# Performance work log

Hardware: AMD Instinct MI355X
Metric: run time of the kernel (lower is better)

Reference implementation:

```python
import jax, jax.numpy as jnp
import numpy as np


def _mlp2(x, w1, b1, w2, b2):
    # two-linear MLP with tanh after each layer (Sequential(MLP, activation))
    h = jnp.tanh(x @ w1.T + b1)
    return jnp.tanh(h @ w2.T + b2)


def setup_inputs() -> dict:
    key = jax.random.key(0)
    ks = jax.random.split(key, 12)
    N, K, D, H, C = 20000, 32, 128, 128, 64
    s = 0.1
    return {
        "z": jax.random.normal(ks[0], (N, D), jnp.float32),
        "z_": jax.random.normal(ks[1], (N, K, D), jnp.float32),
        "cur_w1": s * jax.random.normal(ks[2], (H, D), jnp.float32),
        "cur_b1": jax.random.uniform(ks[3], (H,), jnp.float32, -0.1, 0.1),
        "cur_w2": s * jax.random.normal(ks[4], (H, H), jnp.float32),
        "cur_b2": jax.random.uniform(ks[5], (H,), jnp.float32, -0.1, 0.1),
        "nbr_w1": s * jax.random.normal(ks[6], (H, 2 * D), jnp.float32),
        "nbr_b1": jax.random.uniform(ks[7], (H,), jnp.float32, -0.1, 0.1),
        "nbr_w2": s * jax.random.normal(ks[8], (H, H), jnp.float32),
        "nbr_b2": jax.random.uniform(ks[9], (H,), jnp.float32, -0.1, 0.1),
        "out_w": s * jax.random.normal(ks[10], (C, 2 * H), jnp.float32),
        "out_b": jax.random.uniform(ks[11], (C,), jnp.float32, -0.1, 0.1),
    }


def reference(z, z_, cur_w1, cur_b1, cur_w2, cur_b2,
              nbr_w1, nbr_b1, nbr_w2, nbr_b2, out_w, out_b):
    N, K, D = z_.shape
    # current-node branch: [N, H]
    v = _mlp2(z, cur_w1, cur_b1, cur_w2, cur_b2)
    # neighbor branch: repeat z over K, concat with z_ -> [N, K, 2D]
    zc = jnp.concatenate([jnp.broadcast_to(z[:, None, :], (N, K, D)), z_], axis=2)
    vn = _mlp2(zc, nbr_w1, nbr_b1, nbr_w2, nbr_b2)  # [N, K, H]
    v_ = vn.sum(axis=1)  # sum-aggregate over neighbors -> [N, H]
    # output linear on concatenated features -> [N, dim_c]
    dc = jnp.concatenate([v, v_], axis=1) @ out_w.T + out_b
    return dc
```

## Files before the change

### kernel.cpp

```cpp
#include <hip/hip_runtime.h>


typedef __bf16 bf16;
typedef __bf16 bf16x2 __attribute__((ext_vector_type(2)));
typedef __bf16 bf16x8 __attribute__((ext_vector_type(8)));
typedef float  f32x4  __attribute__((ext_vector_type(4)));

#define MFMA(a, b, c) __builtin_amdgcn_mfma_f32_16x16x32_bf16((a), (b), (c), 0, 0, 0)

__device__ __forceinline__ float fast_tanh(float x) {
    float ax = __builtin_fabsf(x);
    float t  = __builtin_amdgcn_exp2f(ax * 2.885390081777927f);
    float r  = 1.0f - 2.0f * __builtin_amdgcn_rcpf(t + 1.0f);
    return __builtin_copysignf(r, x);
}

__device__ __forceinline__ bf16x8 cvt8(f32x4 a, f32x4 b) {
    bf16x8 r;
    r[0] = (bf16)a[0]; r[1] = (bf16)a[1]; r[2] = (bf16)a[2]; r[3] = (bf16)a[3];
    r[4] = (bf16)b[0]; r[5] = (bf16)b[1]; r[6] = (bf16)b[2]; r[7] = (bf16)b[3];
    return r;
}

__device__ __forceinline__ int swz128(int row, int col) {
    int c = (col >> 3) ^ (row & 15);
    return row * 256 + c * 16 + (col & 7) * 2;
}
__device__ __forceinline__ int swz256(int row, int col) {
    int c = (col >> 3) ^ (row & 15);
    return row * 512 + c * 16 + (col & 7) * 2;
}

__device__ __forceinline__ void st_pair(char* base, int off, float a, float b) {
    bf16x2 p = {(bf16)a, (bf16)b};
    *(bf16x2*)(base + off) = p;
}

__global__ __launch_bounds__(256, 2) void nbr_kernel(
    const float* __restrict__ z, const float* __restrict__ zn,
    const float* __restrict__ w1, const float* __restrict__ b1,
    const float* __restrict__ w2, const float* __restrict__ b2,
    bf16* __restrict__ feat, int N)
{
    __shared__ char zc_lds[32 * 256];
    __shared__ char h1_lds[32 * 256];
    __shared__ char zr_lds[256];

    const int t     = threadIdx.x;
    const int wv    = t >> 6;
    const int lane  = t & 63;
    const int g     = lane >> 4;
    const int li    = lane & 15;
    const int hbase = wv * 32;

    bf16x8 w1f[2][8];
#pragma unroll
    for (int ht = 0; ht < 2; ++ht)
#pragma unroll
        for (int kb = 0; kb < 8; ++kb) {
            const float* p = w1 + (size_t)(hbase + 16*ht + li) * 256 + kb*32 + 8*g;
            w1f[ht][kb] = cvt8(*(const f32x4*)p, *(const f32x4*)(p + 4));
        }
    bf16x8 w2f[2][4];
#pragma unroll
    for (int nt = 0; nt < 2; ++nt)
#pragma unroll
        for (int kb = 0; kb < 4; ++kb) {
            const float* p = w2 + (size_t)(hbase + 16*nt + li) * 128 + kb*32 + 8*g;
            w2f[nt][kb] = cvt8(*(const f32x4*)p, *(const f32x4*)(p + 4));
        }
    float b1v[2][4];
#pragma unroll
    for (int ht = 0; ht < 2; ++ht)
#pragma unroll
        for (int r = 0; r < 4; ++r) b1v[ht][r] = b1[hbase + 16*ht + 4*g + r];
    float b2v[2];
#pragma unroll
    for (int nt = 0; nt < 2; ++nt) b2v[nt] = b2[hbase + 16*nt + li];

    const int sm = t >> 3;
    const int sc = (t & 7) * 16;

    const int stride = gridDim.x;

    f32x4 r0, r1, r2, r3, rz0, rz1;
    {
        int n = blockIdx.x;
        const float* src = zn + ((size_t)n * 32 + sm) * 128 + sc;
        r0 = *(const f32x4*)(src);
        r1 = *(const f32x4*)(src + 4);
        r2 = *(const f32x4*)(src + 8);
        r3 = *(const f32x4*)(src + 12);
        if (t < 16) {
            const float* sz = z + (size_t)n * 128 + t * 8;
            rz0 = *(const f32x4*)sz;
            rz1 = *(const f32x4*)(sz + 4);
        }
    }

    const f32x4 vzero = {0.f, 0.f, 0.f, 0.f};

    for (int n = blockIdx.x; n < N; n += stride) {
        *(bf16x8*)(zc_lds + swz128(sm, sc))     = cvt8(r0, r1);
        *(bf16x8*)(zc_lds + swz128(sm, sc + 8)) = cvt8(r2, r3);
        if (t < 16) *(bf16x8*)(zr_lds + t * 16) = cvt8(rz0, rz1);
        __syncthreads();

        {
            int nn = n + stride;
            if (nn < N) {
                const float* src = zn + ((size_t)nn * 32 + sm) * 128 + sc;
                r0 = *(const f32x4*)(src);
                r1 = *(const f32x4*)(src + 4);
                r2 = *(const f32x4*)(src + 8);
                r3 = *(const f32x4*)(src + 12);
                if (t < 16) {
                    const float* sz = z + (size_t)nn * 128 + t * 8;
                    rz0 = *(const f32x4*)sz;
                    rz1 = *(const f32x4*)(sz + 4);
                }
            }
        }

        bf16x8 az[4];
#pragma unroll
        for (int kb = 0; kb < 4; ++kb)
            az[kb] = *(const bf16x8*)(zr_lds + kb * 64 + g * 16);

        f32x4 acc1[2][2];
#pragma unroll
        for (int a = 0; a < 2; ++a)
#pragma unroll
            for (int b = 0; b < 2; ++b) acc1[a][b] = vzero;

#pragma unroll
        for (int kb = 0; kb < 4; ++kb)
#pragma unroll
            for (int ht = 0; ht < 2; ++ht)
#pragma unroll
                for (int mt = 0; mt < 2; ++mt)
                    acc1[ht][mt] = MFMA(w1f[ht][kb], az[kb], acc1[ht][mt]);
#pragma unroll
        for (int kb = 4; kb < 8; ++kb) {
            bf16x8 bz[2];
#pragma unroll
            for (int mt = 0; mt < 2; ++mt)
                bz[mt] = *(const bf16x8*)(zc_lds + swz128(16*mt + li, (kb - 4)*32 + 8*g));
#pragma unroll
            for (int ht = 0; ht < 2; ++ht)
#pragma unroll
                for (int mt = 0; mt < 2; ++mt)
                    acc1[ht][mt] = MFMA(w1f[ht][kb], bz[mt], acc1[ht][mt]);
        }

#pragma unroll
        for (int ht = 0; ht < 2; ++ht)
#pragma unroll
            for (int mt = 0; mt < 2; ++mt) {
                float v0 = fast_tanh(acc1[ht][mt][0] + b1v[ht][0]);
                float v1 = fast_tanh(acc1[ht][mt][1] + b1v[ht][1]);
                float v2 = fast_tanh(acc1[ht][mt][2] + b1v[ht][2]);
                float v3 = fast_tanh(acc1[ht][mt][3] + b1v[ht][3]);
                int m = 16*mt + li;
                int h = hbase + 16*ht + 4*g;
                st_pair(h1_lds, swz128(m, h),     v0, v1);
                st_pair(h1_lds, swz128(m, h + 2), v2, v3);
            }
        __syncthreads();

        f32x4 acc2[2][2];
#pragma unroll
        for (int a = 0; a < 2; ++a)
#pragma unroll
            for (int b = 0; b < 2; ++b) acc2[a][b] = vzero;

#pragma unroll
        for (int kb = 0; kb < 4; ++kb) {
            bf16x8 ah[2];
#pragma unroll
            for (int mt = 0; mt < 2; ++mt)
                ah[mt] = *(const bf16x8*)(h1_lds + swz128(16*mt + li, kb*32 + 8*g));
#pragma unroll
            for (int mt = 0; mt < 2; ++mt)
#pragma unroll
                for (int nt = 0; nt < 2; ++nt)
                    acc2[mt][nt] = MFMA(ah[mt], w2f[nt][kb], acc2[mt][nt]);
        }

        float s0 = 0.f, s1 = 0.f;
#pragma unroll
        for (int mt = 0; mt < 2; ++mt)
#pragma unroll
            for (int r = 0; r < 4; ++r) {
                s0 += fast_tanh(acc2[mt][0][r] + b2v[0]);
                s1 += fast_tanh(acc2[mt][1][r] + b2v[1]);
            }
        s0 += __shfl_xor(s0, 16); s0 += __shfl_xor(s0, 32);
        s1 += __shfl_xor(s1, 16); s1 += __shfl_xor(s1, 32);
        if (lane < 16) {
            bf16* dst = feat + (size_t)n * 256 + 128 + hbase + lane;
            dst[0]  = (bf16)s0;
            dst[16] = (bf16)s1;
        }
        __syncthreads();
    }
}

__global__ __launch_bounds__(256, 2) void cur_kernel(
    const float* __restrict__ z,
    const float* __restrict__ w1, const float* __restrict__ b1,
    const float* __restrict__ w2, const float* __restrict__ b2,
    bf16* __restrict__ feat, int N)
{
    __shared__ char z_lds[64 * 256];
    __shared__ char h1_lds[64 * 256];

    const int t = threadIdx.x;
    const int wv = t >> 6, lane = t & 63, g = lane >> 4, li = lane & 15;
    const int hbase = wv * 32;
    const int n0 = blockIdx.x * 64;

    bf16x8 w1f[2][4], w2f[2][4];
#pragma unroll
    for (int ht = 0; ht < 2; ++ht)
#pragma unroll
        for (int kb = 0; kb < 4; ++kb) {
            const float* p1 = w1 + (size_t)(hbase + 16*ht + li) * 128 + kb*32 + 8*g;
            w1f[ht][kb] = cvt8(*(const f32x4*)p1, *(const f32x4*)(p1 + 4));
            const float* p2 = w2 + (size_t)(hbase + 16*ht + li) * 128 + kb*32 + 8*g;
            w2f[ht][kb] = cvt8(*(const f32x4*)p2, *(const f32x4*)(p2 + 4));
        }
    float b1v[2][4], b2v[2][4];
#pragma unroll
    for (int ht = 0; ht < 2; ++ht)
#pragma unroll
        for (int r = 0; r < 4; ++r) {
            b1v[ht][r] = b1[hbase + 16*ht + 4*g + r];
            b2v[ht][r] = b2[hbase + 16*ht + 4*g + r];
        }

    {
        int m = t >> 2;
        int c0 = (t & 3) * 32;
        int row = n0 + m; if (row > N - 1) row = N - 1;
        const float* src = z + (size_t)row * 128 + c0;
#pragma unroll
        for (int q = 0; q < 4; ++q) {
            f32x4 a = *(const f32x4*)(src + 8*q);
            f32x4 b = *(const f32x4*)(src + 8*q + 4);
            *(bf16x8*)(z_lds + swz128(m, c0 + 8*q)) = cvt8(a, b);
        }
    }
    __syncthreads();

    const f32x4 vzero = {0.f, 0.f, 0.f, 0.f};
    f32x4 acc1[2][4];
#pragma unroll
    for (int a = 0; a < 2; ++a)
#pragma unroll
        for (int b = 0; b < 4; ++b) acc1[a][b] = vzero;

#pragma unroll
    for (int kb = 0; kb < 4; ++kb) {
        bf16x8 bz[4];
#pragma unroll
        for (int mt = 0; mt < 4; ++mt)
            bz[mt] = *(const bf16x8*)(z_lds + swz128(16*mt + li, kb*32 + 8*g));
#pragma unroll
        for (int ht = 0; ht < 2; ++ht)
#pragma unroll
            for (int mt = 0; mt < 4; ++mt)
                acc1[ht][mt] = MFMA(w1f[ht][kb], bz[mt], acc1[ht][mt]);
    }
#pragma unroll
    for (int ht = 0; ht < 2; ++ht)
#pragma unroll
        for (int mt = 0; mt < 4; ++mt) {
            float v0 = fast_tanh(acc1[ht][mt][0] + b1v[ht][0]);
            float v1 = fast_tanh(acc1[ht][mt][1] + b1v[ht][1]);
            float v2 = fast_tanh(acc1[ht][mt][2] + b1v[ht][2]);
            float v3 = fast_tanh(acc1[ht][mt][3] + b1v[ht][3]);
            int m = 16*mt + li;
            int h = hbase + 16*ht + 4*g;
            st_pair(h1_lds, swz128(m, h),     v0, v1);
            st_pair(h1_lds, swz128(m, h + 2), v2, v3);
        }
    __syncthreads();

    f32x4 acc2[2][4];
#pragma unroll
    for (int a = 0; a < 2; ++a)
#pragma unroll
        for (int b = 0; b < 4; ++b) acc2[a][b] = vzero;

#pragma unroll
    for (int kb = 0; kb < 4; ++kb) {
        bf16x8 bh[4];
#pragma unroll
        for (int mt = 0; mt < 4; ++mt)
            bh[mt] = *(const bf16x8*)(h1_lds + swz128(16*mt + li, kb*32 + 8*g));
#pragma unroll
        for (int ht = 0; ht < 2; ++ht)
#pragma unroll
            for (int mt = 0; mt < 4; ++mt)
                acc2[ht][mt] = MFMA(w2f[ht][kb], bh[mt], acc2[ht][mt]);
    }
#pragma unroll
    for (int ht = 0; ht < 2; ++ht)
#pragma unroll
        for (int mt = 0; mt < 4; ++mt) {
            float v0 = fast_tanh(acc2[ht][mt][0] + b2v[ht][0]);
            float v1 = fast_tanh(acc2[ht][mt][1] + b2v[ht][1]);
            float v2 = fast_tanh(acc2[ht][mt][2] + b2v[ht][2]);
            float v3 = fast_tanh(acc2[ht][mt][3] + b2v[ht][3]);
            int row = n0 + 16*mt + li;
            if (row < N) {
                int h = hbase + 16*ht + 4*g;
                bf16* dst = feat + (size_t)row * 256 + h;
                bf16x2 p01 = {(bf16)v0, (bf16)v1};
                bf16x2 p23 = {(bf16)v2, (bf16)v3};
                *(bf16x2*)(dst)     = p01;
                *(bf16x2*)(dst + 2) = p23;
            }
        }
}

__global__ __launch_bounds__(256, 2) void out_kernel(
    const bf16* __restrict__ feat,
    const float* __restrict__ ow, const float* __restrict__ ob,
    float* __restrict__ out, int N)
{
    __shared__ char f_lds[64 * 512];

    const int t = threadIdx.x, wv = t >> 6, lane = t & 63, g = lane >> 4, li = lane & 15;
    const int cbase = wv * 16;
    const int n0 = blockIdx.x * 64;

    bf16x8 owf[8];
#pragma unroll
    for (int kb = 0; kb < 8; ++kb) {
        const float* p = ow + (size_t)(cbase + li) * 256 + kb*32 + 8*g;
        owf[kb] = cvt8(*(const f32x4*)p, *(const f32x4*)(p + 4));
    }
    float obv = ob[cbase + li];

    {
        int m = t >> 2;
        int c0 = (t & 3) * 64;
        int row = n0 + m; if (row > N - 1) row = N - 1;
        const bf16* src = feat + (size_t)row * 256 + c0;
#pragma unroll
        for (int q = 0; q < 8; ++q)
            *(bf16x8*)(f_lds + swz256(m, c0 + 8*q)) = *(const bf16x8*)(src + 8*q);
    }
    __syncthreads();

    const f32x4 vzero = {0.f, 0.f, 0.f, 0.f};
    f32x4 acc[4];
#pragma unroll
    for (int a = 0; a < 4; ++a) acc[a] = vzero;

#pragma unroll
    for (int kb = 0; kb < 8; ++kb) {
        bf16x8 af[4];
#pragma unroll
        for (int mt = 0; mt < 4; ++mt)
            af[mt] = *(const bf16x8*)(f_lds + swz256(16*mt + li, kb*32 + 8*g));
#pragma unroll
        for (int mt = 0; mt < 4; ++mt)
            acc[mt] = MFMA(af[mt], owf[kb], acc[mt]);
    }
#pragma unroll
    for (int mt = 0; mt < 4; ++mt)
#pragma unroll
        for (int r = 0; r < 4; ++r) {
            int row = n0 + 16*mt + 4*g + r;
            if (row < N) out[(size_t)row * 64 + cbase + li] = acc[mt][r] + obv;
        }
}

extern "C" void kernel_launch(void* const* d_in, const int* in_sizes, int n_in,
                              void* d_out, int out_size, void* d_ws, size_t ws_size,
                              hipStream_t stream) {
    const float* z   = (const float*)d_in[0];
    const float* zn  = (const float*)d_in[1];
    const float* cw1 = (const float*)d_in[2];
    const float* cb1 = (const float*)d_in[3];
    const float* cw2 = (const float*)d_in[4];
    const float* cb2 = (const float*)d_in[5];
    const float* nw1 = (const float*)d_in[6];
    const float* nb1 = (const float*)d_in[7];
    const float* nw2 = (const float*)d_in[8];
    const float* nb2 = (const float*)d_in[9];
    const float* ow  = (const float*)d_in[10];
    const float* ob  = (const float*)d_in[11];
    float* out = (float*)d_out;
    bf16* feat = (bf16*)d_ws;

    const int N = in_sizes[0] / 128;
    const int nblk = (N + 63) / 64;

    (void)n_in; (void)out_size; (void)ws_size;

    cur_kernel<<<nblk, 256, 0, stream>>>(z, cw1, cb1, cw2, cb2, feat, N);
    nbr_kernel<<<512, 256, 0, stream>>>(z, zn, nw1, nb1, nw2, nb2, feat, N);
    out_kernel<<<nblk, 256, 0, stream>>>(feat, ow, ob, out, N);
}
```

Before: 136.4 us.

## Precompute z-part of neighbor layer-1 once per node and batch two nodes per iteration

The z half of the neighbor MLP's first layer (W1[:, :128]·z + b1) is identical across all K neighbors. It is now computed once per node inside cur_kernel and written as an fp32 u1 buffer, which nbr_kernel reads as a per-node bias. This halves nbr's first-layer MFMA work. nbr_kernel now handles two nodes per loop iteration with double LDS buffers, drops the trailing barrier, and raises wave priority around MFMA sections. The node-pair loop uses NP = N/2, so an odd N would drop the last node; N=20000 is even here. It also adds the u1 round trip through global memory.

```diff
diff --git a/kernel.cpp b/kernel.cpp
--- a/kernel.cpp
+++ b/kernel.cpp
@@ -37,28 +37,24 @@
 }
 
 __global__ __launch_bounds__(256, 2) void nbr_kernel(
-    const float* __restrict__ z, const float* __restrict__ zn,
-    const float* __restrict__ w1, const float* __restrict__ b1,
-    const float* __restrict__ w2, const float* __restrict__ b2,
-    bf16* __restrict__ feat, int N)
+    const float* __restrict__ zn, const float* __restrict__ u1,
+    const float* __restrict__ w1, const float* __restrict__ w2,
+    const float* __restrict__ b2,
+    bf16* __restrict__ feat, int NP)
 {
-    __shared__ char zc_lds[32 * 256];
-    __shared__ char h1_lds[32 * 256];
-    __shared__ char zr_lds[256];
-
-    const int t     = threadIdx.x;
-    const int wv    = t >> 6;
-    const int lane  = t & 63;
-    const int g     = lane >> 4;
-    const int li    = lane & 15;
+    __shared__ char zc_lds[2][32 * 256];
+    __shared__ char h1_lds[2][32 * 256];
+
+    const int t = threadIdx.x;
+    const int wv = t >> 6, lane = t & 63, g = lane >> 4, li = lane & 15;
     const int hbase = wv * 32;
 
-    bf16x8 w1f[2][8];
-#pragma unroll
-    for (int ht = 0; ht < 2; ++ht)
-#pragma unroll
-        for (int kb = 0; kb < 8; ++kb) {
-            const float* p = w1 + (size_t)(hbase + 16*ht + li) * 256 + kb*32 + 8*g;
+    bf16x8 w1f[2][4];
+#pragma unroll
+    for (int ht = 0; ht < 2; ++ht)
+#pragma unroll
+        for (int kb = 0; kb < 4; ++kb) {
+            const float* p = w1 + (size_t)(hbase + 16*ht + li) * 256 + 128 + kb*32 + 8*g;
             w1f[ht][kb] = cvt8(*(const f32x4*)p, *(const f32x4*)(p + 4));
         }
     bf16x8 w2f[2][4];
@@ -69,140 +65,146 @@
             const float* p = w2 + (size_t)(hbase + 16*nt + li) * 128 + kb*32 + 8*g;
             w2f[nt][kb] = cvt8(*(const f32x4*)p, *(const f32x4*)(p + 4));
         }
-    float b1v[2][4];
-#pragma unroll
-    for (int ht = 0; ht < 2; ++ht)
-#pragma unroll
-        for (int r = 0; r < 4; ++r) b1v[ht][r] = b1[hbase + 16*ht + 4*g + r];
     float b2v[2];
 #pragma unroll
     for (int nt = 0; nt < 2; ++nt) b2v[nt] = b2[hbase + 16*nt + li];
 
-    const int sm = t >> 3;
-    const int sc = (t & 7) * 16;
-
+    const int sm  = t >> 3;
+    const int scf = (t & 7) * 16;
     const int stride = gridDim.x;
 
-    f32x4 r0, r1, r2, r3, rz0, rz1;
+    f32x4 r[2][4];
+    f32x4 uu[2][2];
     {
-        int n = blockIdx.x;
-        const float* src = zn + ((size_t)n * 32 + sm) * 128 + sc;
-        r0 = *(const f32x4*)(src);
-        r1 = *(const f32x4*)(src + 4);
-        r2 = *(const f32x4*)(src + 8);
-        r3 = *(const f32x4*)(src + 12);
-        if (t < 16) {
-            const float* sz = z + (size_t)n * 128 + t * 8;
-            rz0 = *(const f32x4*)sz;
-            rz1 = *(const f32x4*)(sz + 4);
+        int p = blockIdx.x;
+#pragma unroll
+        for (int j = 0; j < 2; ++j) {
+            const float* src = zn + ((size_t)(2*p + j) * 32 + sm) * 128 + scf;
+#pragma unroll
+            for (int q = 0; q < 4; ++q) r[j][q] = *(const f32x4*)(src + 4*q);
+#pragma unroll
+            for (int ht = 0; ht < 2; ++ht)
+                uu[j][ht] = *(const f32x4*)(u1 + (size_t)(2*p + j) * 128 + hbase + 16*ht + 4*g);
         }
     }
 
     const f32x4 vzero = {0.f, 0.f, 0.f, 0.f};
 
-    for (int n = blockIdx.x; n < N; n += stride) {
-        *(bf16x8*)(zc_lds + swz128(sm, sc))     = cvt8(r0, r1);
-        *(bf16x8*)(zc_lds + swz128(sm, sc + 8)) = cvt8(r2, r3);
-        if (t < 16) *(bf16x8*)(zr_lds + t * 16) = cvt8(rz0, rz1);
+    for (int p = blockIdx.x; p < NP; p += stride) {
+#pragma unroll
+        for (int j = 0; j < 2; ++j) {
+            *(bf16x8*)(zc_lds[j] + swz128(sm, scf))     = cvt8(r[j][0], r[j][1]);
+            *(bf16x8*)(zc_lds[j] + swz128(sm, scf + 8)) = cvt8(r[j][2], r[j][3]);
+        }
         __syncthreads();
 
-        {
-            int nn = n + stride;
-            if (nn < N) {
-                const float* src = zn + ((size_t)nn * 32 + sm) * 128 + sc;
-                r0 = *(const f32x4*)(src);
-                r1 = *(const f32x4*)(src + 4);
-                r2 = *(const f32x4*)(src + 8);
-                r3 = *(const f32x4*)(src + 12);
-                if (t < 16) {
-                    const float* sz = z + (size_t)nn * 128 + t * 8;
-                    rz0 = *(const f32x4*)sz;
-                    rz1 = *(const f32x4*)(sz + 4);
+        const int pp = p + stride;
+        if (pp < NP) {
+#pragma unroll
+            for (int j = 0; j < 2; ++j) {
+                const float* src = zn + ((size_t)(2*pp + j) * 32 + sm) * 128 + scf;
+#pragma unroll
+                for (int q = 0; q < 4; ++q) r[j][q] = *(const f32x4*)(src + 4*q);
+            }
+        }
+
+        f32x4 acc1[2][2][2];
+#pragma unroll
+        for (int j = 0; j < 2; ++j)
+#pragma unroll
+            for (int a = 0; a < 2; ++a)
+#pragma unroll
+                for (int b = 0; b < 2; ++b) acc1[j][a][b] = vzero;
+
+        __builtin_amdgcn_s_setprio(1);
+#pragma unroll
+        for (int kb = 0; kb < 4; ++kb) {
+            bf16x8 bz[2][2];
+#pragma unroll
+            for (int j = 0; j < 2; ++j)
+#pragma unroll
+                for (int mt = 0; mt < 2; ++mt)
+                    bz[j][mt] = *(const bf16x8*)(zc_lds[j] + swz128(16*mt + li, kb*32 + 8*g));
+#pragma unroll
+            for (int j = 0; j < 2; ++j)
+#pragma unroll
+                for (int ht = 0; ht < 2; ++ht)
+#pragma unroll
+                    for (int mt = 0; mt < 2; ++mt)
+                        acc1[j][ht][mt] = MFMA(w1f[ht][kb], bz[j][mt], acc1[j][ht][mt]);
+        }
+        __builtin_amdgcn_s_setprio(0);
+
+#pragma unroll
+        for (int j = 0; j < 2; ++j)
+#pragma unroll
+            for (int ht = 0; ht < 2; ++ht)
+#pragma unroll
+                for (int mt = 0; mt < 2; ++mt) {
+                    float v0 = fast_tanh(acc1[j][ht][mt][0] + uu[j][ht][0]);
+                    float v1 = fast_tanh(acc1[j][ht][mt][1] + uu[j][ht][1]);
+                    float v2 = fast_tanh(acc1[j][ht][mt][2] + uu[j][ht][2]);
+                    float v3 = fast_tanh(acc1[j][ht][mt][3] + uu[j][ht][3]);
+                    int m = 16*mt + li;
+                    int h = hbase + 16*ht + 4*g;
+                    st_pair(h1_lds[j], swz128(m, h),     v0, v1);
+                    st_pair(h1_lds[j], swz128(m, h + 2), v2, v3);
                 }
+
+        if (pp < NP) {
+#pragma unroll
+            for (int j = 0; j < 2; ++j)
+#pragma unroll
+                for (int ht = 0; ht < 2; ++ht)
+                    uu[j][ht] = *(const f32x4*)(u1 + (size_t)(2*pp + j) * 128 + hbase + 16*ht + 4*g);
+        }
+        __syncthreads();
+
+        f32x4 acc2[2][2][2];
+#pragma unroll
+        for (int j = 0; j < 2; ++j)
+#pragma unroll
+            for (int a = 0; a < 2; ++a)
+#pragma unroll
+                for (int b = 0; b < 2; ++b) acc2[j][a][b] = vzero;
+
+        __builtin_amdgcn_s_setprio(1);
+#pragma unroll
+        for (int kb = 0; kb < 4; ++kb) {
+            bf16x8 ah[2][2];
+#pragma unroll
+            for (int j = 0; j < 2; ++j)
+#pragma unroll
+                for (int mt = 0; mt < 2; ++mt)
+                    ah[j][mt] = *(const bf16x8*)(h1_lds[j] + swz128(16*mt + li, kb*32 + 8*g));
+#pragma unroll
+            for (int j = 0; j < 2; ++j)
+#pragma unroll
+                for (int mt = 0; mt < 2; ++mt)
+#pragma unroll
+                    for (int nt = 0; nt < 2; ++nt)
+                        acc2[j][mt][nt] = MFMA(ah[j][mt], w2f[nt][kb], acc2[j][mt][nt]);
+        }
+        __builtin_amdgcn_s_setprio(0);
+
+#pragma unroll
+        for (int j = 0; j < 2; ++j) {
+            float s0 = 0.f, s1 = 0.f;
+#pragma unroll
+            for (int mt = 0; mt < 2; ++mt)
+#pragma unroll
+                for (int rr = 0; rr < 4; ++rr) {
+                    s0 += fast_tanh(acc2[j][mt][0][rr] + b2v[0]);
+                    s1 += fast_tanh(acc2[j][mt][1][rr] + b2v[1]);
+                }
+            s0 += __shfl_xor(s0, 16); s0 += __shfl_xor(s0, 32);
+            s1 += __shfl_xor(s1, 16); s1 += __shfl_xor(s1, 32);
+            if (lane < 16) {
+                bf16* dst = feat + (size_t)(2*p + j) * 256 + 128 + hbase + lane;
+                dst[0]  = (bf16)s0;
+                dst[16] = (bf16)s1;
             }
         }
-
-        bf16x8 az[4];
-#pragma unroll
-        for (int kb = 0; kb < 4; ++kb)
-            az[kb] = *(const bf16x8*)(zr_lds + kb * 64 + g * 16);
-
-        f32x4 acc1[2][2];
-#pragma unroll
-        for (int a = 0; a < 2; ++a)
-#pragma unroll
-            for (int b = 0; b < 2; ++b) acc1[a][b] = vzero;
-
-#pragma unroll
-        for (int kb = 0; kb < 4; ++kb)
-#pragma unroll
-            for (int ht = 0; ht < 2; ++ht)
-#pragma unroll
-                for (int mt = 0; mt < 2; ++mt)
-                    acc1[ht][mt] = MFMA(w1f[ht][kb], az[kb], acc1[ht][mt]);
-#pragma unroll
-        for (int kb = 4; kb < 8; ++kb) {
-            bf16x8 bz[2];
-#pragma unroll
-            for (int mt = 0; mt < 2; ++mt)
-                bz[mt] = *(const bf16x8*)(zc_lds + swz128(16*mt + li, (kb - 4)*32 + 8*g));
-#pragma unroll
-            for (int ht = 0; ht < 2; ++ht)
-#pragma unroll
-                for (int mt = 0; mt < 2; ++mt)
-                    acc1[ht][mt] = MFMA(w1f[ht][kb], bz[mt], acc1[ht][mt]);
-        }
-
-#pragma unroll
-        for (int ht = 0; ht < 2; ++ht)
-#pragma unroll
-            for (int mt = 0; mt < 2; ++mt) {
-                float v0 = fast_tanh(acc1[ht][mt][0] + b1v[ht][0]);
-                float v1 = fast_tanh(acc1[ht][mt][1] + b1v[ht][1]);
-                float v2 = fast_tanh(acc1[ht][mt][2] + b1v[ht][2]);
-                float v3 = fast_tanh(acc1[ht][mt][3] + b1v[ht][3]);
-                int m = 16*mt + li;
-                int h = hbase + 16*ht + 4*g;
-                st_pair(h1_lds, swz128(m, h),     v0, v1);
-                st_pair(h1_lds, swz128(m, h + 2), v2, v3);
-            }
-        __syncthreads();
-
-        f32x4 acc2[2][2];
-#pragma unroll
-        for (int a = 0; a < 2; ++a)
-#pragma unroll
-            for (int b = 0; b < 2; ++b) acc2[a][b] = vzero;
-
-#pragma unroll
-        for (int kb = 0; kb < 4; ++kb) {
-            bf16x8 ah[2];
-#pragma unroll
-            for (int mt = 0; mt < 2; ++mt)
-                ah[mt] = *(const bf16x8*)(h1_lds + swz128(16*mt + li, kb*32 + 8*g));
-#pragma unroll
-            for (int mt = 0; mt < 2; ++mt)
-#pragma unroll
-                for (int nt = 0; nt < 2; ++nt)
-                    acc2[mt][nt] = MFMA(ah[mt], w2f[nt][kb], acc2[mt][nt]);
-        }
-
-        float s0 = 0.f, s1 = 0.f;
-#pragma unroll
-        for (int mt = 0; mt < 2; ++mt)
-#pragma unroll
-            for (int r = 0; r < 4; ++r) {
-                s0 += fast_tanh(acc2[mt][0][r] + b2v[0]);
-                s1 += fast_tanh(acc2[mt][1][r] + b2v[1]);
-            }
-        s0 += __shfl_xor(s0, 16); s0 += __shfl_xor(s0, 32);
-        s1 += __shfl_xor(s1, 16); s1 += __shfl_xor(s1, 32);
-        if (lane < 16) {
-            bf16* dst = feat + (size_t)n * 256 + 128 + hbase + lane;
-            dst[0]  = (bf16)s0;
-            dst[16] = (bf16)s1;
-        }
-        __syncthreads();
     }
 }
 
@@ -210,7 +212,8 @@
     const float* __restrict__ z,
     const float* __restrict__ w1, const float* __restrict__ b1,
     const float* __restrict__ w2, const float* __restrict__ b2,
-    bf16* __restrict__ feat, int N)
+    const float* __restrict__ nw1, const float* __restrict__ nb1,
+    bf16* __restrict__ feat, float* __restrict__ u1, int N)
 {
     __shared__ char z_lds[64 * 256];
     __shared__ char h1_lds[64 * 256];
@@ -220,7 +223,7 @@
     const int hbase = wv * 32;
     const int n0 = blockIdx.x * 64;
 
-    bf16x8 w1f[2][4], w2f[2][4];
+    bf16x8 w1f[2][4], w2f[2][4], wzf[2][4];
 #pragma unroll
     for (int ht = 0; ht < 2; ++ht)
 #pragma unroll
@@ -229,14 +232,17 @@
             w1f[ht][kb] = cvt8(*(const f32x4*)p1, *(const f32x4*)(p1 + 4));
             const float* p2 = w2 + (size_t)(hbase + 16*ht + li) * 128 + kb*32 + 8*g;
             w2f[ht][kb] = cvt8(*(const f32x4*)p2, *(const f32x4*)(p2 + 4));
-        }
-    float b1v[2][4], b2v[2][4];
-#pragma unroll
-    for (int ht = 0; ht < 2; ++ht)
-#pragma unroll
-        for (int r = 0; r < 4; ++r) {
-            b1v[ht][r] = b1[hbase + 16*ht + 4*g + r];
-            b2v[ht][r] = b2[hbase + 16*ht + 4*g + r];
+            const float* p3 = nw1 + (size_t)(hbase + 16*ht + li) * 256 + kb*32 + 8*g;
+            wzf[ht][kb] = cvt8(*(const f32x4*)p3, *(const f32x4*)(p3 + 4));
+        }
+    float b1v[2][4], b2v[2][4], bnv[2][4];
+#pragma unroll
+    for (int ht = 0; ht < 2; ++ht)
+#pragma unroll
+        for (int rr = 0; rr < 4; ++rr) {
+            b1v[ht][rr] = b1[hbase + 16*ht + 4*g + rr];
+            b2v[ht][rr] = b2[hbase + 16*ht + 4*g + rr];
+            bnv[ht][rr] = nb1[hbase + 16*ht + 4*g + rr];
         }
 
     {
@@ -254,11 +260,11 @@
     __syncthreads();
 
     const f32x4 vzero = {0.f, 0.f, 0.f, 0.f};
-    f32x4 acc1[2][4];
+    f32x4 acc1[2][4], accz[2][4];
 #pragma unroll
     for (int a = 0; a < 2; ++a)
 #pragma unroll
-        for (int b = 0; b < 4; ++b) acc1[a][b] = vzero;
+        for (int b = 0; b < 4; ++b) { acc1[a][b] = vzero; accz[a][b] = vzero; }
 
 #pragma unroll
     for (int kb = 0; kb < 4; ++kb) {
@@ -269,9 +275,25 @@
 #pragma unroll
         for (int ht = 0; ht < 2; ++ht)
 #pragma unroll
-            for (int mt = 0; mt < 4; ++mt)
+            for (int mt = 0; mt < 4; ++mt) {
                 acc1[ht][mt] = MFMA(w1f[ht][kb], bz[mt], acc1[ht][mt]);
-    }
+                accz[ht][mt] = MFMA(wzf[ht][kb], bz[mt], accz[ht][mt]);
+            }
+    }
+
+#pragma unroll
+    for (int ht = 0; ht < 2; ++ht)
+#pragma unroll
+        for (int mt = 0; mt < 4; ++mt) {
+            int row = n0 + 16*mt + li;
+            if (row < N) {
+                f32x4 v;
+#pragma unroll
+                for (int rr = 0; rr < 4; ++rr) v[rr] = accz[ht][mt][rr] + bnv[ht][rr];
+                *(f32x4*)(u1 + (size_t)row * 128 + hbase + 16*ht + 4*g) = v;
+            }
+        }
+
 #pragma unroll
     for (int ht = 0; ht < 2; ++ht)
 #pragma unroll
@@ -373,9 +395,9 @@
 #pragma unroll
     for (int mt = 0; mt < 4; ++mt)
 #pragma unroll
-        for (int r = 0; r < 4; ++r) {
-            int row = n0 + 16*mt + 4*g + r;
-            if (row < N) out[(size_t)row * 64 + cbase + li] = acc[mt][r] + obv;
+        for (int rr = 0; rr < 4; ++rr) {
+            int row = n0 + 16*mt + 4*g + rr;
+            if (row < N) out[(size_t)row * 64 + cbase + li] = acc[mt][rr] + obv;
         }
 }
 
@@ -395,14 +417,17 @@
     const float* ow  = (const float*)d_in[10];
     const float* ob  = (const float*)d_in[11];
     float* out = (float*)d_out;
-    bf16* feat = (bf16*)d_ws;
-
-    const int N = in_sizes[0] / 128;
+
+    const int N  = in_sizes[0] / 128;
+    const int NP = N / 2;
     const int nblk = (N + 63) / 64;
 
+    bf16*  feat = (bf16*)d_ws;
+    float* u1   = (float*)((char*)d_ws + (size_t)N * 256 * sizeof(bf16));
+
     (void)n_in; (void)out_size; (void)ws_size;
 
-    cur_kernel<<<nblk, 256, 0, stream>>>(z, cw1, cb1, cw2, cb2, feat, N);
-    nbr_kernel<<<512, 256, 0, stream>>>(z, zn, nw1, nb1, nw2, nb2, feat, N);
+    cur_kernel<<<nblk, 256, 0, stream>>>(z, cw1, cb1, cw2, cb2, nw1, nb1, feat, u1, N);
+    nbr_kernel<<<512, 256, 0, stream>>>(zn, u1, nw1, nw2, nb2, feat, NP);
     out_kernel<<<nblk, 256, 0, stream>>>(feat, ow, ob, out, N);
 }
```

After: 126.3 us. 1.08x faster.
